# Performance work log

Hardware: AMD Instinct MI355X
Metric: run time of the kernel (lower is better)

The kernel has to match this reference:

```python
import jax, jax.numpy as jnp
import numpy as np

GROUPS = 32
EPS = 1e-6


def group_norm(x, gamma, beta):
    b, h, w, c = x.shape
    xg = x.reshape(b, h, w, GROUPS, c // GROUPS)
    mean = jnp.mean(xg, axis=(1, 2, 4), keepdims=True)
    var = jnp.var(xg, axis=(1, 2, 4), keepdims=True)
    xg = (xg - mean) * jax.lax.rsqrt(var + EPS)
    return xg.reshape(b, h, w, c) * gamma + beta


def setup_inputs() -> dict:
    key = jax.random.key(0)
    ks = jax.random.split(key, 6)
    B, H, W, C = 4, 64, 64, 512
    scale = 0.02
    return {
        "x": jax.random.normal(ks[0], (B, H, W, C), dtype=jnp.float32),
        "gamma": jnp.ones((C,), dtype=jnp.float32),
        "beta": jnp.zeros((C,), dtype=jnp.float32),
        "wq": jax.random.normal(ks[1], (C, C), dtype=jnp.float32) * scale,
        "bq": jnp.zeros((C,), dtype=jnp.float32),
        "wk": jax.random.normal(ks[2], (C, C), dtype=jnp.float32) * scale,
        "bk": jnp.zeros((C,), dtype=jnp.float32),
        "wv": jax.random.normal(ks[3], (C, C), dtype=jnp.float32) * scale,
        "bv": jnp.zeros((C,), dtype=jnp.float32),
        "wo": jax.random.normal(ks[4], (C, C), dtype=jnp.float32) * scale,
        "bo": jnp.zeros((C,), dtype=jnp.float32),
    }


def reference(x, gamma, beta, wq, bq, wk, bk, wv, bv, wo, bo):
    b, h, w, c = x.shape
    xn = group_norm(x, gamma, beta)
    # 1x1 convs == per-pixel linear layers
    q = (jnp.einsum('bhwc,cd->bhwd', xn, wq) + bq).reshape(b, h * w, c)
    k = (jnp.einsum('bhwc,cd->bhwd', xn, wk) + bk).reshape(b, h * w, c)
    v = (jnp.einsum('bhwc,cd->bhwd', xn, wv) + bv).reshape(b, h * w, c)
    # full (hw x hw) attention, single head
    scores = jnp.einsum('bic,bjc->bij', q, k) * (c ** -0.5)  # [b, hw, hw]
    attn = jax.nn.softmax(scores, axis=-1)
    out = jnp.einsum('bij,bjc->bic', attn, v).reshape(b, h, w, c)
    return jnp.einsum('bhwc,cd->bhwd', out, wo) + bo + x
```

## Files before the change

kernel.cpp:

```cpp
#include <hip/hip_runtime.h>
#include <stdint.h>


typedef __attribute__((ext_vector_type(8))) short bf16x8;
typedef __attribute__((ext_vector_type(8))) unsigned short u16x8;
typedef __attribute__((ext_vector_type(4))) float f32x4;

#define QSCALE 0.06376237087058025f

__device__ __forceinline__ unsigned short f2bf(float f) {
  unsigned int x = __float_as_uint(f);
  x += 0x7fffu + ((x >> 16) & 1u);
  return (unsigned short)(x >> 16);
}
__device__ __forceinline__ float bf2f(unsigned short u) {
  return __uint_as_float((unsigned int)u << 16);
}

__device__ __forceinline__ void gl_lds16(const void* g, void* l) {
  __builtin_amdgcn_global_load_lds(
      (__attribute__((address_space(1))) unsigned char*)g,
      (__attribute__((address_space(3))) unsigned char*)l, 16, 0, 0);
}

#define SBAR() asm volatile("s_barrier" ::: "memory")

__device__ __forceinline__ void gemm_tile(
    const unsigned short* __restrict__ A, long lda,
    const unsigned short* __restrict__ B, long ldb,
    int K,
    unsigned short* As0, unsigned short* As1,
    unsigned short* Bs0, unsigned short* Bs1,
    f32x4 acc[4][4]) {
  const int tid = threadIdx.x;
  const int wave = tid >> 6, lane = tid & 63;
  const int srow = lane >> 3;
  const int gg = lane & 7;
  const int wm = (wave >> 1) * 64, wn = (wave & 1) * 64;
  const int lrow = lane & 15;
  const int rsw = lrow & 7;
  const int kgb = lane >> 4;

  auto STAGE = [&](unsigned short* as, unsigned short* bs, int k0) {
#pragma unroll
    for (int i = 0; i < 4; ++i) {
      int chunk = wave * 4 + i;
      int row = chunk * 8 + srow;
      int soffA = (gg ^ srow) * 16;
      int soffB = (gg ^ ((chunk * 2 + (srow >> 2)) & 7)) * 16;
      gl_lds16((const char*)(A + (long)row * lda + k0) + soffA, (char*)as + chunk * 1024);
      gl_lds16((const char*)(B + (long)row * ldb + k0) + soffB, (char*)bs + chunk * 1024);
    }
  };

  auto COMPUTE = [&](const unsigned short* as, const unsigned short* bs) {
#pragma unroll
    for (int ks = 0; ks < 2; ++ks) {
      bf16x8 af[4], bfr[4];
      const int off = ((ks * 4 + kgb) ^ rsw) * 8;
#pragma unroll
      for (int t = 0; t < 4; ++t) {
        af[t]  = *(const bf16x8*)&as[(wm + t * 16 + lrow) * 64 + off];
        bfr[t] = *(const bf16x8*)&bs[(wn + 4 * lrow + t) * 64 + off];
      }
#pragma unroll
      for (int mt = 0; mt < 4; ++mt)
#pragma unroll
        for (int nt = 0; nt < 4; ++nt)
          acc[mt][nt] = __builtin_amdgcn_mfma_f32_16x16x32_bf16(af[mt], bfr[nt], acc[mt][nt], 0, 0, 0);
    }
  };

  const int nk = K >> 6;
  STAGE(As0, Bs0, 0);
  __syncthreads();
  for (int t = 0; t < nk; t += 2) {
    if (t + 1 < nk) STAGE(As1, Bs1, (t + 1) * 64);
    COMPUTE(As0, Bs0);
    __syncthreads();
    if (t + 2 < nk) STAGE(As0, Bs0, (t + 2) * 64);
    COMPUTE(As1, Bs1);
    __syncthreads();
  }
}

#define GEMM_SHARED                                              \
  __shared__ unsigned short As0[128 * 64], As1[128 * 64];        \
  __shared__ unsigned short Bs0[128 * 64], Bs1[128 * 64];

#define EPILOG_SETUP                                          \
  const int lane = threadIdx.x & 63, wave = threadIdx.x >> 6; \
  const int wm = (wave >> 1) * 64, wn = (wave & 1) * 64;      \
  const int lcol4 = (lane & 15) * 4, lrb = (lane >> 4) * 4;

__device__ __forceinline__ void gemm256_tile(
    const unsigned short* __restrict__ A, long lda,
    const unsigned short* __restrict__ B, long ldb,
    int NT, unsigned short* lds, f32x4 acc[8][4]) {
  const int tid = threadIdx.x;
  const int wave = tid >> 6, lane = tid & 63;
  const int wm = wave >> 2, wn = wave & 3;
  const int lrow = lane & 15, kgb = lane >> 4;
  const int koff = (kgb ^ ((lrow >> 1) & 3)) * 8;
  const int srow = wave * 32 + (lane >> 2);
  const int sg = ((lane & 3) ^ ((lane >> 3) & 3)) * 8;
  const int sdst = wave * 1024;

  auto STAGE = [&](int t, int kh, int isB) {
    const unsigned short* src = (isB ? B : A) + (long)t * 64 + kh * 32 + sg;
    long ld = isB ? ldb : lda;
    unsigned short* db = lds + isB * 32768 + ((t & 1) * 2 + kh) * 8192 + sdst;
    gl_lds16(src + (long)srow * ld, db);
    gl_lds16(src + (long)(srow + 16) * ld, db + 512);
  };

  STAGE(0, 0, 0); STAGE(0, 0, 1);
  STAGE(0, 1, 0); STAGE(0, 1, 1);
  STAGE(1, 0, 0); STAGE(1, 0, 1);

  for (int T = 0; T < NT; ++T) {
    const int d2 = (T & 1) * 2;
    const unsigned short* aB = lds + d2 * 8192 + (wm * 128 + lrow) * 32 + koff;
    const unsigned short* bB = lds + 32768 + d2 * 8192 + ((wn & 1) * 64 + lrow) * 32 + koff;
    const bool more = (T + 1 < NT);
    bf16x8 a0[4], a1[4], b0[4];

    if (more) { asm volatile("s_waitcnt vmcnt(8)" ::: "memory"); }
    else      { asm volatile("s_waitcnt vmcnt(4)" ::: "memory"); }
    SBAR();

#pragma unroll
    for (int m = 0; m < 4; ++m) a0[m] = *(const bf16x8*)(aB + m * 512);
#pragma unroll
    for (int n = 0; n < 4; ++n) b0[n] = *(const bf16x8*)(bB + n * 512);
    if (more) STAGE(T + 1, 1, 0);
    SBAR();
    __builtin_amdgcn_s_setprio(1);
#pragma unroll
    for (int m = 0; m < 4; ++m)
#pragma unroll
      for (int n = 0; n < 4; ++n)
        acc[m][n] = __builtin_amdgcn_mfma_f32_16x16x32_bf16(a0[m], b0[n], acc[m][n], 0, 0, 0);
    __builtin_amdgcn_s_setprio(0);

#pragma unroll
    for (int m = 0; m < 4; ++m) a1[m] = *(const bf16x8*)(aB + (4 + m) * 512);
    if (more) STAGE(T + 1, 1, 1);
    SBAR();
    __builtin_amdgcn_s_setprio(1);
#pragma unroll
    for (int m = 0; m < 4; ++m)
#pragma unroll
      for (int n = 0; n < 4; ++n)
        acc[4 + m][n] = __builtin_amdgcn_mfma_f32_16x16x32_bf16(a1[m], b0[n], acc[4 + m][n], 0, 0, 0);
    __builtin_amdgcn_s_setprio(0);

    if (more) { asm volatile("s_waitcnt vmcnt(8)" ::: "memory"); }
    else      { asm volatile("s_waitcnt vmcnt(0)" ::: "memory"); }
    SBAR();

    const unsigned short* aB1 = aB + 8192;
    const unsigned short* bB1 = bB + 8192;
#pragma unroll
    for (int m = 0; m < 4; ++m) a0[m] = *(const bf16x8*)(aB1 + m * 512);
#pragma unroll
    for (int n = 0; n < 4; ++n) b0[n] = *(const bf16x8*)(bB1 + n * 512);
    if (T + 2 < NT) STAGE(T + 2, 0, 0);
    SBAR();
    __builtin_amdgcn_s_setprio(1);
#pragma unroll
    for (int m = 0; m < 4; ++m)
#pragma unroll
      for (int n = 0; n < 4; ++n)
        acc[m][n] = __builtin_amdgcn_mfma_f32_16x16x32_bf16(a0[m], b0[n], acc[m][n], 0, 0, 0);
    __builtin_amdgcn_s_setprio(0);
    SBAR();

#pragma unroll
    for (int m = 0; m < 4; ++m) a1[m] = *(const bf16x8*)(aB1 + (4 + m) * 512);
    if (T + 2 < NT) STAGE(T + 2, 0, 1);
    SBAR();
    __builtin_amdgcn_s_setprio(1);
#pragma unroll
    for (int m = 0; m < 4; ++m)
#pragma unroll
      for (int n = 0; n < 4; ++n)
        acc[4 + m][n] = __builtin_amdgcn_mfma_f32_16x16x32_bf16(a1[m], b0[n], acc[4 + m][n], 0, 0, 0);
    __builtin_amdgcn_s_setprio(0);
  }
}

__global__ void prep_kernel(const float* __restrict__ wq, const float* __restrict__ wk,
                            const float* __restrict__ wv, const float* __restrict__ wo,
                            const float* __restrict__ bq, const float* __restrict__ bk,
                            const float* __restrict__ bv,
                            unsigned short* __restrict__ wqkvT,
                            unsigned short* __restrict__ woT,
                            float* __restrict__ bias, float* __restrict__ stats,
                            float* __restrict__ lsum) {
  long id = (long)blockIdx.x * 256 + threadIdx.x;
  if (id < 786432) {
    long n = id >> 9, k = id & 511;
    const float* w = (n < 512) ? wq : (n < 1024 ? wk : wv);
    wqkvT[id] = f2bf(w[k * 512 + (n & 511)]);
  } else if (id < 786432 + 262144) {
    long j = id - 786432, n = j >> 9, k = j & 511;
    woT[j] = f2bf(wo[k * 512 + n]);
  } else if (id < 786432 + 262144 + 1536) {
    long j = id - 786432 - 262144;
    bias[j] = (j < 512) ? bq[j] : (j < 1024 ? bk[j - 512] : bv[j - 1024]);
  } else if (id < 786432 + 262144 + 1536 + 256) {
    stats[id - 786432 - 262144 - 1536] = 0.f;
  } else if (id < 786432 + 262144 + 1536 + 256 + 16384) {
    lsum[id - 786432 - 262144 - 1536 - 256] = 0.f;
  }
}

__global__ __launch_bounds__(256) void gn_stats(const float* __restrict__ x,
                                                float* __restrict__ stats) {
  const int b = blockIdx.x >> 7, slab = blockIdx.x & 127;
  const float* xp = x + (long)b * 4096 * 512 + (long)slab * 32 * 512;
  const int tid = threadIdx.x;
  float s = 0.f, s2 = 0.f;
  for (int it = 0; it < 16; ++it) {
    int i = it * 256 + tid;
    float4 v = *(const float4*)(xp + (long)i * 4);
    s += v.x + v.y + v.z + v.w;
    s2 += v.x * v.x + v.y * v.y + v.z * v.z + v.w * v.w;
  }
  s += __shfl_xor(s, 1); s += __shfl_xor(s, 2);
  s2 += __shfl_xor(s2, 1); s2 += __shfl_xor(s2, 2);
  if ((tid & 3) == 0) {
    int g = (tid & 127) >> 2;
    atomicAdd(&stats[(b * 32 + g) * 2], s);
    atomicAdd(&stats[(b * 32 + g) * 2 + 1], s2);
  }
}

__global__ __launch_bounds__(256) void gn_apply(const float* __restrict__ x,
                                                const float* __restrict__ stats,
                                                const float* __restrict__ gamma,
                                                const float* __restrict__ beta,
                                                unsigned short* __restrict__ xn) {
  long id = (long)blockIdx.x * 256 + threadIdx.x;
  long a = id * 4;
  int b = (int)(id >> 19);
  int ch = (int)(a & 511);
  int g = ch >> 4;
  float s = stats[(b * 32 + g) * 2], s2 = stats[(b * 32 + g) * 2 + 1];
  float mean = s * (1.f / 65536.f);
  float rinv = rsqrtf(s2 * (1.f / 65536.f) - mean * mean + 1e-6f);
  float4 v = *(const float4*)(x + a);
  float4 gm = *(const float4*)(gamma + ch);
  float4 bt = *(const float4*)(beta + ch);
  ushort4 o;
  o.x = f2bf((v.x - mean) * rinv * gm.x + bt.x);
  o.y = f2bf((v.y - mean) * rinv * gm.y + bt.y);
  o.z = f2bf((v.z - mean) * rinv * gm.z + bt.z);
  o.w = f2bf((v.w - mean) * rinv * gm.w + bt.w);
  *(ushort4*)(xn + a) = o;
}

__global__ __launch_bounds__(512, 2) void qkv_kernel(
    const unsigned short* __restrict__ xn, const unsigned short* __restrict__ wqkvT,
    const float* __restrict__ bias, unsigned short* __restrict__ q,
    unsigned short* __restrict__ kk, unsigned short* __restrict__ vv) {
  __shared__ unsigned short lds[65536];
  f32x4 acc[8][4] = {};
  const long tm = (long)blockIdx.x * 256, tn = (long)blockIdx.y * 256;
  gemm256_tile(xn + tm * 512, 512, wqkvT + tn * 512, 512, 8, lds, acc);
  const int lane = threadIdx.x & 63, wave = threadIdx.x >> 6;
  const int wm2 = wave >> 2, wn4 = wave & 3;
  const int lcol = lane & 15, lrb = (lane >> 4) * 4;
  const int region = (int)(tn >> 9);
  unsigned short* dst = region == 0 ? q : (region == 1 ? kk : vv);
  const float sc = region == 0 ? QSCALE : 1.f;
  float bv[4];
#pragma unroll
  for (int nf = 0; nf < 4; ++nf) bv[nf] = bias[tn + wn4 * 64 + nf * 16 + lcol];
#pragma unroll
  for (int mf = 0; mf < 8; ++mf)
#pragma unroll
    for (int nf = 0; nf < 4; ++nf) {
      long n = tn + wn4 * 64 + nf * 16 + lcol;
      long nloc = n & 511;
#pragma unroll
      for (int r = 0; r < 4; ++r) {
        long m = tm + wm2 * 128 + mf * 16 + lrb + r;
        dst[m * 512 + nloc] = f2bf((acc[mf][nf][r] + bv[nf]) * sc);
      }
    }
}

__global__ __launch_bounds__(256) void transpose_v(const unsigned short* __restrict__ v,
                                                   unsigned short* __restrict__ vT) {
  const int b = blockIdx.z;
  const long j0 = (long)blockIdx.x * 64, c0 = (long)blockIdx.y * 64;
  __shared__ unsigned short t[64][72];
  const int tc = (threadIdx.x & 15) * 4, tr = threadIdx.x >> 4;
  for (int rr = 0; rr < 64; rr += 16) {
    ushort4 u = *(const ushort4*)&v[((long)b * 4096 + j0 + tr + rr) * 512 + c0 + tc];
    t[tr + rr][tc] = u.x; t[tr + rr][tc + 1] = u.y;
    t[tr + rr][tc + 2] = u.z; t[tr + rr][tc + 3] = u.w;
  }
  __syncthreads();
  for (int rr = 0; rr < 64; rr += 16) {
    int c = tr + rr;
    ushort4 o;
    o.x = t[tc + 0][c]; o.y = t[tc + 1][c]; o.z = t[tc + 2][c]; o.w = t[tc + 3][c];
    *(ushort4*)&vT[((long)b * 512 + c0 + c) * 4096 + j0 + tc] = o;
  }
}

__global__ __launch_bounds__(256) void qkt_kernel(
    const unsigned short* __restrict__ q, const unsigned short* __restrict__ kk,
    unsigned short* __restrict__ probs, float* __restrict__ lsum, int b0) {
  GEMM_SHARED
  f32x4 acc[4][4] = {};
  const int z = blockIdx.z;
  const long bb = (long)(b0 + z) * 4096 * 512;
  const long tm = (long)blockIdx.x * 128, tn = (long)blockIdx.y * 128;
  gemm_tile(q + bb + tm * 512, 512, kk + bb + tn * 512, 512, 512, As0, As1, Bs0, Bs1, acc);
  EPILOG_SETUP
  unsigned short* out = probs + (long)z * 4096 * 4096;
  float* ls = lsum + (long)(b0 + z) * 4096;
  const long n0 = tn + wn + lcol4;
#pragma unroll
  for (int mt = 0; mt < 4; ++mt) {
    float rs[4];
#pragma unroll
    for (int r = 0; r < 4; ++r) {
      float e0 = exp2f(acc[mt][0][r]);
      float e1 = exp2f(acc[mt][1][r]);
      float e2 = exp2f(acc[mt][2][r]);
      float e3 = exp2f(acc[mt][3][r]);
      rs[r] = (e0 + e1) + (e2 + e3);
      ushort4 o;
      o.x = f2bf(e0); o.y = f2bf(e1); o.z = f2bf(e2); o.w = f2bf(e3);
      long m = tm + wm + mt * 16 + lrb + r;
      *(ushort4*)&out[m * 4096 + n0] = o;
    }
#pragma unroll
    for (int r = 0; r < 4; ++r) {
      float s = rs[r];
      s += __shfl_xor(s, 1); s += __shfl_xor(s, 2);
      s += __shfl_xor(s, 4); s += __shfl_xor(s, 8);
      if (lcol4 == 0) atomicAdd(&ls[tm + wm + mt * 16 + lrb + r], s);
    }
  }
}

__global__ __launch_bounds__(256) void pv_kernel(
    const unsigned short* __restrict__ probs, const unsigned short* __restrict__ vT,
    const float* __restrict__ lsum, unsigned short* __restrict__ attn, int b0) {
  GEMM_SHARED
  f32x4 acc[4][4] = {};
  const int z = blockIdx.z;
  const long tm = (long)blockIdx.x * 128, tn = (long)blockIdx.y * 128;
  gemm_tile(probs + (long)z * 4096 * 4096 + tm * 4096, 4096,
            vT + (long)(b0 + z) * 512 * 4096 + tn * 4096, 4096,
            4096, As0, As1, Bs0, Bs1, acc);
  EPILOG_SETUP
  unsigned short* out = attn + (long)(b0 + z) * 4096 * 512;
  const float* ls = lsum + (long)(b0 + z) * 4096;
  const long n0 = tn + wn + lcol4;
#pragma unroll
  for (int mt = 0; mt < 4; ++mt)
#pragma unroll
    for (int r = 0; r < 4; ++r) {
      long m = tm + wm + mt * 16 + lrb + r;
      float inv = __builtin_amdgcn_rcpf(ls[m]);
      ushort4 o;
      o.x = f2bf(acc[mt][0][r] * inv); o.y = f2bf(acc[mt][1][r] * inv);
      o.z = f2bf(acc[mt][2][r] * inv); o.w = f2bf(acc[mt][3][r] * inv);
      *(ushort4*)&out[m * 512 + n0] = o;
    }
}

__global__ __launch_bounds__(256) void proj_kernel(
    const unsigned short* __restrict__ attn, const unsigned short* __restrict__ woT,
    const float* __restrict__ bo, const float* __restrict__ x,
    float* __restrict__ out) {
  GEMM_SHARED
  f32x4 acc[4][4] = {};
  const long tm = (long)blockIdx.x * 128, tn = (long)blockIdx.y * 128;
  gemm_tile(attn + tm * 512, 512, woT + tn * 512, 512, 512, As0, As1, Bs0, Bs1, acc);
  EPILOG_SETUP
  const long n0 = tn + wn + lcol4;
  float4 bs = *(const float4*)&bo[n0];
#pragma unroll
  for (int mt = 0; mt < 4; ++mt)
#pragma unroll
    for (int r = 0; r < 4; ++r) {
      long m = tm + wm + mt * 16 + lrb + r;
      float4 xv = *(const float4*)&x[m * 512 + n0];
      float4 o;
      o.x = acc[mt][0][r] + bs.x + xv.x;
      o.y = acc[mt][1][r] + bs.y + xv.y;
      o.z = acc[mt][2][r] + bs.z + xv.z;
      o.w = acc[mt][3][r] + bs.w + xv.w;
      *(float4*)&((float*)out)[m * 512 + n0] = o;
    }
}

extern "C" void kernel_launch(void* const* d_in, const int* in_sizes, int n_in,
                              void* d_out, int out_size, void* d_ws, size_t ws_size,
                              hipStream_t stream) {
  const float* x     = (const float*)d_in[0];
  const float* gamma = (const float*)d_in[1];
  const float* beta  = (const float*)d_in[2];
  const float* wq    = (const float*)d_in[3];
  const float* bq    = (const float*)d_in[4];
  const float* wk    = (const float*)d_in[5];
  const float* bk    = (const float*)d_in[6];
  const float* wv    = (const float*)d_in[7];
  const float* bv    = (const float*)d_in[8];
  const float* wo    = (const float*)d_in[9];
  const float* bo    = (const float*)d_in[10];

  char* p = (char*)d_ws;
  auto take = [&](size_t bytes) { char* r = p; p += (bytes + 255) & ~(size_t)255; return r; };
  const long NTOK = 16384, C = 512, HW = 4096;
  unsigned short* xn    = (unsigned short*)take(NTOK * C * 2);
  unsigned short* q     = (unsigned short*)take(NTOK * C * 2);
  unsigned short* kbuf  = (unsigned short*)take(NTOK * C * 2);
  unsigned short* vT    = (unsigned short*)take(NTOK * C * 2);
  unsigned short* wqkvT = (unsigned short*)take(1536l * 512 * 2);
  unsigned short* woT   = (unsigned short*)take(512l * 512 * 2);
  float* bias           = (float*)take(1536 * 4);
  float* stats          = (float*)take(256 * 4);
  float* lsum           = (float*)take(16384 * 4);

  size_t fixed = (size_t)(p - (char*)d_ws);
  size_t per_nb = (size_t)HW * HW * 2 + 512;
  int NB = (ws_size >= fixed + 4 * per_nb) ? 4
         : (ws_size >= fixed + 2 * per_nb) ? 2 : 1;
  unsigned short* probs = (unsigned short*)take((size_t)NB * HW * HW * 2);
  unsigned short* attn  = xn;
  unsigned short* vbuf  = probs;

  prep_kernel<<<4168, 256, 0, stream>>>(wq, wk, wv, wo, bq, bk, bv, wqkvT, woT,
                                        bias, stats, lsum);
  gn_stats<<<512, 256, 0, stream>>>(x, stats);
  gn_apply<<<8192, 256, 0, stream>>>(x, stats, gamma, beta, xn);

  qkv_kernel<<<dim3(64, 6), 512, 0, stream>>>(xn, wqkvT, bias, q, kbuf, vbuf);
  transpose_v<<<dim3(64, 8, 4), 256, 0, stream>>>(vbuf, vT);

  for (int b0 = 0; b0 < 4; b0 += NB) {
    qkt_kernel<<<dim3(32, 32, NB), 256, 0, stream>>>(q, kbuf, probs, lsum, b0);
    pv_kernel<<<dim3(32, 4, NB), 256, 0, stream>>>(probs, vT, lsum, attn, b0);
  }

  proj_kernel<<<dim3(128, 4), 256, 0, stream>>>(attn, woT, bo, x, (float*)d_out);
}
```

Before: 361.0 us.

## Fuse V transpose into QKV epilogue and merge prep with GN stats

The QKV GEMM epilogue now writes V directly in transposed layout using 4-element vector stores, which removes the separate transpose_v kernel and its extra round trip through memory. The weight prep kernel and the group-norm statistics kernel are combined into one launch by splitting on block index. Zeroing of stats and lsum moves to a hipMemsetAsync that relies on the two buffers being adjacent in the workspace. The result is fewer launches and less traffic, at the cost of V stores that are strided across rows in the GEMM epilogue.

```diff
diff --git a/kernel.cpp b/kernel.cpp
--- a/kernel.cpp
+++ b/kernel.cpp
@@ -3,7 +3,6 @@
 
 
 typedef __attribute__((ext_vector_type(8))) short bf16x8;
-typedef __attribute__((ext_vector_type(8))) unsigned short u16x8;
 typedef __attribute__((ext_vector_type(4))) float f32x4;
 
 #define QSCALE 0.06376237087058025f
@@ -190,35 +189,30 @@
   }
 }
 
-__global__ void prep_kernel(const float* __restrict__ wq, const float* __restrict__ wk,
-                            const float* __restrict__ wv, const float* __restrict__ wo,
-                            const float* __restrict__ bq, const float* __restrict__ bk,
-                            const float* __restrict__ bv,
-                            unsigned short* __restrict__ wqkvT,
-                            unsigned short* __restrict__ woT,
-                            float* __restrict__ bias, float* __restrict__ stats,
-                            float* __restrict__ lsum) {
-  long id = (long)blockIdx.x * 256 + threadIdx.x;
-  if (id < 786432) {
-    long n = id >> 9, k = id & 511;
-    const float* w = (n < 512) ? wq : (n < 1024 ? wk : wv);
-    wqkvT[id] = f2bf(w[k * 512 + (n & 511)]);
-  } else if (id < 786432 + 262144) {
-    long j = id - 786432, n = j >> 9, k = j & 511;
-    woT[j] = f2bf(wo[k * 512 + n]);
-  } else if (id < 786432 + 262144 + 1536) {
-    long j = id - 786432 - 262144;
-    bias[j] = (j < 512) ? bq[j] : (j < 1024 ? bk[j - 512] : bv[j - 1024]);
-  } else if (id < 786432 + 262144 + 1536 + 256) {
-    stats[id - 786432 - 262144 - 1536] = 0.f;
-  } else if (id < 786432 + 262144 + 1536 + 256 + 16384) {
-    lsum[id - 786432 - 262144 - 1536 - 256] = 0.f;
-  }
-}
-
-__global__ __launch_bounds__(256) void gn_stats(const float* __restrict__ x,
-                                                float* __restrict__ stats) {
-  const int b = blockIdx.x >> 7, slab = blockIdx.x & 127;
+__global__ __launch_bounds__(256) void prep_gn(
+    const float* __restrict__ wq, const float* __restrict__ wk,
+    const float* __restrict__ wv, const float* __restrict__ wo,
+    const float* __restrict__ bq, const float* __restrict__ bk,
+    const float* __restrict__ bv, const float* __restrict__ x,
+    unsigned short* __restrict__ wqkvT, unsigned short* __restrict__ woT,
+    float* __restrict__ bias, float* __restrict__ stats) {
+  if (blockIdx.x < 4102) {
+    long id = (long)blockIdx.x * 256 + threadIdx.x;
+    if (id < 786432) {
+      long n = id >> 9, k = id & 511;
+      const float* w = (n < 512) ? wq : (n < 1024 ? wk : wv);
+      wqkvT[id] = f2bf(w[k * 512 + (n & 511)]);
+    } else if (id < 786432 + 262144) {
+      long j = id - 786432, n = j >> 9, k = j & 511;
+      woT[j] = f2bf(wo[k * 512 + n]);
+    } else {
+      long j = id - 786432 - 262144;
+      bias[j] = (j < 512) ? bq[j] : (j < 1024 ? bk[j - 512] : bv[j - 1024]);
+    }
+    return;
+  }
+  const int bI = blockIdx.x - 4102;
+  const int b = bI >> 7, slab = bI & 127;
   const float* xp = x + (long)b * 4096 * 512 + (long)slab * 32 * 512;
   const int tid = threadIdx.x;
   float s = 0.f, s2 = 0.f;
@@ -264,7 +258,7 @@
 __global__ __launch_bounds__(512, 2) void qkv_kernel(
     const unsigned short* __restrict__ xn, const unsigned short* __restrict__ wqkvT,
     const float* __restrict__ bias, unsigned short* __restrict__ q,
-    unsigned short* __restrict__ kk, unsigned short* __restrict__ vv) {
+    unsigned short* __restrict__ kk, unsigned short* __restrict__ vT) {
   __shared__ unsigned short lds[65536];
   f32x4 acc[8][4] = {};
   const long tm = (long)blockIdx.x * 256, tn = (long)blockIdx.y * 256;
@@ -273,42 +267,38 @@
   const int wm2 = wave >> 2, wn4 = wave & 3;
   const int lcol = lane & 15, lrb = (lane >> 4) * 4;
   const int region = (int)(tn >> 9);
-  unsigned short* dst = region == 0 ? q : (region == 1 ? kk : vv);
-  const float sc = region == 0 ? QSCALE : 1.f;
   float bv[4];
 #pragma unroll
   for (int nf = 0; nf < 4; ++nf) bv[nf] = bias[tn + wn4 * 64 + nf * 16 + lcol];
-#pragma unroll
-  for (int mf = 0; mf < 8; ++mf)
-#pragma unroll
-    for (int nf = 0; nf < 4; ++nf) {
-      long n = tn + wn4 * 64 + nf * 16 + lcol;
-      long nloc = n & 511;
-#pragma unroll
-      for (int r = 0; r < 4; ++r) {
-        long m = tm + wm2 * 128 + mf * 16 + lrb + r;
-        dst[m * 512 + nloc] = f2bf((acc[mf][nf][r] + bv[nf]) * sc);
+  if (region < 2) {
+    unsigned short* dst = region == 0 ? q : kk;
+    const float sc = region == 0 ? QSCALE : 1.f;
+#pragma unroll
+    for (int mf = 0; mf < 8; ++mf)
+#pragma unroll
+      for (int nf = 0; nf < 4; ++nf) {
+        long nloc = (tn + wn4 * 64 + nf * 16 + lcol) & 511;
+#pragma unroll
+        for (int r = 0; r < 4; ++r) {
+          long m = tm + wm2 * 128 + mf * 16 + lrb + r;
+          dst[m * 512 + nloc] = f2bf((acc[mf][nf][r] + bv[nf]) * sc);
+        }
       }
-    }
-}
-
-__global__ __launch_bounds__(256) void transpose_v(const unsigned short* __restrict__ v,
-                                                   unsigned short* __restrict__ vT) {
-  const int b = blockIdx.z;
-  const long j0 = (long)blockIdx.x * 64, c0 = (long)blockIdx.y * 64;
-  __shared__ unsigned short t[64][72];
-  const int tc = (threadIdx.x & 15) * 4, tr = threadIdx.x >> 4;
-  for (int rr = 0; rr < 64; rr += 16) {
-    ushort4 u = *(const ushort4*)&v[((long)b * 4096 + j0 + tr + rr) * 512 + c0 + tc];
-    t[tr + rr][tc] = u.x; t[tr + rr][tc + 1] = u.y;
-    t[tr + rr][tc + 2] = u.z; t[tr + rr][tc + 3] = u.w;
-  }
-  __syncthreads();
-  for (int rr = 0; rr < 64; rr += 16) {
-    int c = tr + rr;
-    ushort4 o;
-    o.x = t[tc + 0][c]; o.y = t[tc + 1][c]; o.z = t[tc + 2][c]; o.w = t[tc + 3][c];
-    *(ushort4*)&vT[((long)b * 512 + c0 + c) * 4096 + j0 + tc] = o;
+  } else {
+#pragma unroll
+    for (int mf = 0; mf < 8; ++mf)
+#pragma unroll
+      for (int nf = 0; nf < 4; ++nf) {
+        long c = (tn + wn4 * 64 + nf * 16 + lcol) - 1024;
+        long m = tm + wm2 * 128 + mf * 16 + lrb;
+        long b = m >> 12, j = m & 4095;
+        ushort4 o;
+        o.x = f2bf(acc[mf][nf][0] + bv[nf]);
+        o.y = f2bf(acc[mf][nf][1] + bv[nf]);
+        o.z = f2bf(acc[mf][nf][2] + bv[nf]);
+        o.w = f2bf(acc[mf][nf][3] + bv[nf]);
+        *(ushort4*)&vT[(b * 512 + c) * 4096 + j] = o;
+      }
   }
 }
 
@@ -437,15 +427,14 @@
          : (ws_size >= fixed + 2 * per_nb) ? 2 : 1;
   unsigned short* probs = (unsigned short*)take((size_t)NB * HW * HW * 2);
   unsigned short* attn  = xn;
-  unsigned short* vbuf  = probs;
-
-  prep_kernel<<<4168, 256, 0, stream>>>(wq, wk, wv, wo, bq, bk, bv, wqkvT, woT,
-                                        bias, stats, lsum);
-  gn_stats<<<512, 256, 0, stream>>>(x, stats);
+
+  hipMemsetAsync(stats, 0, 1024 + 16384 * 4, stream);
+
+  prep_gn<<<4614, 256, 0, stream>>>(wq, wk, wv, wo, bq, bk, bv, x,
+                                    wqkvT, woT, bias, stats);
   gn_apply<<<8192, 256, 0, stream>>>(x, stats, gamma, beta, xn);
 
-  qkv_kernel<<<dim3(64, 6), 512, 0, stream>>>(xn, wqkvT, bias, q, kbuf, vbuf);
-  transpose_v<<<dim3(64, 8, 4), 256, 0, stream>>>(vbuf, vT);
+  qkv_kernel<<<dim3(64, 6), 512, 0, stream>>>(xn, wqkvT, bias, q, kbuf, vT);
 
   for (int b0 = 0; b0 < 4; b0 += NB) {
     qkt_kernel<<<dim3(32, 32, NB), 256, 0, stream>>>(q, kbuf, probs, lsum, b0);
```

After: 353.2 us. 2.2% less time.
